# Kernel optimization log

Measured on AMD Instinct MI355X. Metric: run time of the kernel, lower is better.

The kernel has to match this reference:

```python
import jax, jax.numpy as jnp
import numpy as np

D_MODEL = 1024
HEADS = 16
D_HEAD = D_MODEL // HEADS


def setup_inputs() -> dict:
    key = jax.random.key(0)
    ks = jax.random.split(key, 5)
    B, S = 4, 2048
    x = jax.random.normal(ks[0], (B, S, D_MODEL), dtype=jnp.float32)
    # nn.Linear weights are [out, in]; store as [in, out] for x @ W convention
    s_qkv = 1.0 / np.sqrt(D_MODEL)
    w_qkv = jax.random.uniform(ks[1], (D_MODEL, 3 * D_MODEL), jnp.float32, -s_qkv, s_qkv)
    b_qkv = jax.random.uniform(ks[2], (3 * D_MODEL,), jnp.float32, -s_qkv, s_qkv)
    w_proj = jax.random.uniform(ks[3], (D_MODEL, D_MODEL), jnp.float32, -s_qkv, s_qkv)
    b_proj = jax.random.uniform(ks[4], (D_MODEL,), jnp.float32, -s_qkv, s_qkv)
    return {"x": x, "w_qkv": w_qkv, "b_qkv": b_qkv, "w_proj": w_proj, "b_proj": b_proj}


def reference(x, w_qkv, b_qkv, w_proj, b_proj):
    B, S, D = x.shape
    scale = D_HEAD ** (-0.5)
    qkv = x @ w_qkv + b_qkv                        # [B,S,3D]
    qkv = qkv.reshape(B, S, 3, HEADS, D_HEAD)
    qkv = jnp.transpose(qkv, (2, 0, 3, 1, 4))      # [3,B,H,S,dh]
    q, k, v = qkv[0], qkv[1], qkv[2]
    attn = jnp.einsum("bhsd,bhtd->bhst", q, k) * scale
    attn = jax.nn.softmax(attn, axis=-1)
    ctx = jnp.einsum("bhst,bhtd->bhsd", attn, v)   # [B,H,S,dh]
    ctx = jnp.transpose(ctx, (0, 2, 1, 3)).reshape(B, S, D)
    return ctx @ w_proj + b_proj
```

## Files before the change

### kernel.cpp

```cpp
#include <hip/hip_runtime.h>

typedef unsigned short u16;
typedef unsigned int u32;
typedef __attribute__((ext_vector_type(8))) short short8;
typedef __attribute__((ext_vector_type(4))) float f32x4;
typedef __attribute__((ext_vector_type(2))) unsigned int u32x2;

extern "C" __device__ float __ocml_native_exp2_f32(float);

__device__ __forceinline__ u16 f32_to_bf16(float f) {
  u32 u = __builtin_bit_cast(u32, f);
  u += 0x7fffu + ((u >> 16) & 1u);
  return (u16)(u >> 16);
}

__device__ __forceinline__ u32 cvt_pk_bf16(float a, float b) {
  u32 r;
  asm("v_cvt_pk_bf16_f32 %0, %1, %2" : "=v"(r) : "v"(a), "v"(b));
  return r;
}

__device__ __forceinline__ void gload16(const void* g, void* l) {
  __builtin_amdgcn_global_load_lds((const __attribute__((address_space(1))) u32*)g,
                                   (__attribute__((address_space(3))) u32*)l, 16, 0, 0);
}

__global__ __launch_bounds__(256) void prep_kernel(const float* __restrict__ x,
                                                   u16* __restrict__ xb,
                                                   const float* __restrict__ w_qkv,
                                                   u16* __restrict__ wqkvT,
                                                   const float* __restrict__ w_proj,
                                                   u16* __restrict__ wprojT) {
  __shared__ u16 tile[32][33];
  const int bid = blockIdx.x, tid = threadIdx.x;
  if (bid < 4096) {
    int i = bid * 256 + tid;
    const float4* p = (const float4*)x + (size_t)i * 2;
    float4 a = p[0], b = p[1];
    int4 v;
    v.x = (int)f32_to_bf16(a.x) | ((int)f32_to_bf16(a.y) << 16);
    v.y = (int)f32_to_bf16(a.z) | ((int)f32_to_bf16(a.w) << 16);
    v.z = (int)f32_to_bf16(b.x) | ((int)f32_to_bf16(b.y) << 16);
    v.w = (int)f32_to_bf16(b.z) | ((int)f32_to_bf16(b.w) << 16);
    *(int4*)(xb + (size_t)i * 8) = v;
    return;
  }
  const float* in;
  u16* out;
  int bx, by, C;
  if (bid < 7168) {
    int t = bid - 4096;
    bx = t % 96; by = t / 96; C = 3072; in = w_qkv; out = wqkvT;
  } else {
    int t = bid - 7168;
    bx = t % 32; by = t / 32; C = 1024; in = w_proj; out = wprojT;
  }
  const int R = 1024;
  int tx = tid & 31, ty = tid >> 5;
  int c0 = bx * 32, r0 = by * 32;
#pragma unroll
  for (int j = 0; j < 32; j += 8)
    tile[ty + j][tx] = f32_to_bf16(in[(size_t)(r0 + ty + j) * C + c0 + tx]);
  __syncthreads();
#pragma unroll
  for (int j = 0; j < 32; j += 8)
    out[(size_t)(c0 + ty + j) * R + r0 + tx] = tile[tx][ty + j];
}

__global__ __launch_bounds__(512, 2) void gemm256_kernel(
    const u16* __restrict__ A, const u16* __restrict__ Bt, const float* __restrict__ bias,
    u16* __restrict__ qo, u16* __restrict__ ko, u16* __restrict__ vo) {
  __shared__ u16 lds[2][2][2][8192];
  const int tid = threadIdx.x;
  const int lane = tid & 63, w = tid >> 6;
  const int lo = lane & 15, hi = lane >> 4;
  const int wr = w >> 2, wn4 = w & 3;
  const int id = blockIdx.y * gridDim.x + blockIdx.x;
  const int swz = (id & 7) * 48 + (id >> 3);
  const int bn = (swz % 12) * 256, bm = (swz / 12) * 256;
  const int srow4 = lane >> 2;
  const int scol = (lane & 3) ^ ((lane >> 3) & 3);
  const u16* aRow = A + (size_t)(bm + w * 16 + srow4) * 1024 + scol * 8;
  const u16* bRow = Bt + (size_t)(bn + w * 16 + srow4) * 1024 + scol * 8;
  const int achk = (hi ^ ((lo >> 1) & 3)) * 8;
  const int bro = wn4 * 64;

  f32x4 acc[8][4] = {};

#define STG(sdb, sab, shk, tile)                                      \
  if ((tile) < 16) {                                                  \
    const u16* g = ((sab) ? bRow : aRow) + (tile) * 64 + (shk) * 32;  \
    u16* d = &lds[sdb][sab][shk][w * 512];                            \
    gload16(g, d);                                                    \
    gload16(g + 128 * 1024, d + 4096);                                \
  }

#define W8 asm volatile("s_waitcnt vmcnt(8)" ::: "memory")
#define W4 asm volatile("s_waitcnt vmcnt(4)" ::: "memory")
#define W0 asm volatile("s_waitcnt vmcnt(0)" ::: "memory")
#define WN ((void)0)

  STG(0, 0, 0, 0); STG(0, 1, 0, 0); STG(0, 0, 1, 0); STG(0, 1, 1, 0);
  STG(1, 0, 0, 1); STG(1, 1, 0, 1);
  W8;
  __builtin_amdgcn_s_barrier();

#define PHASE(db, MH, KK, sdb, sab, shk, tile, WAITOP)                                           \
  {                                                                                              \
    short8 af[4], bf[4];                                                                         \
    _Pragma("unroll") for (int m4 = 0; m4 < 4; ++m4)                                             \
      af[m4] = *(const short8*)&lds[db][0][KK][(wr * 128 + MH * 64 + m4 * 16 + lo) * 32 + achk]; \
    _Pragma("unroll") for (int ni = 0; ni < 4; ++ni)                                             \
      bf[ni] = *(const short8*)&lds[db][1][KK][(bro + ni * 16 + lo) * 32 + achk];                \
    STG(sdb, sab, shk, tile);                                                                    \
    WAITOP;                                                                                      \
    __builtin_amdgcn_s_barrier();                                                                \
    asm volatile("s_waitcnt lgkmcnt(0)" ::: "memory");                                           \
    __builtin_amdgcn_sched_barrier(0);                                                           \
    __builtin_amdgcn_s_setprio(1);                                                               \
    _Pragma("unroll") for (int m4 = 0; m4 < 4; ++m4)                                             \
      _Pragma("unroll") for (int ni = 0; ni < 4; ++ni)                                           \
        acc[MH * 4 + m4][ni] = __builtin_amdgcn_mfma_f32_16x16x32_bf16(                          \
            af[m4], bf[ni], acc[MH * 4 + m4][ni], 0, 0, 0);                                      \
    __builtin_amdgcn_s_setprio(0);                                                               \
    __builtin_amdgcn_s_barrier();                                                                \
  }

  for (int i = 0; i < 7; ++i) {
    const int t1 = 2 * i + 1, t2 = 2 * i + 2, t3 = 2 * i + 3;
    PHASE(0, 0, 0, 1, 0, 1, t1, WN);
    PHASE(0, 1, 0, 1, 1, 1, t1, W8);
    PHASE(0, 0, 1, 0, 0, 0, t2, WN);
    PHASE(0, 1, 1, 0, 1, 0, t2, W8);
    PHASE(1, 0, 0, 0, 0, 1, t2, WN);
    PHASE(1, 1, 0, 0, 1, 1, t2, W8);
    PHASE(1, 0, 1, 1, 0, 0, t3, WN);
    PHASE(1, 1, 1, 1, 1, 0, t3, W8);
  }
  PHASE(0, 0, 0, 1, 0, 1, 15, WN);
  PHASE(0, 1, 0, 1, 1, 1, 15, W8);
  PHASE(0, 0, 1, 0, 0, 0, 16, WN);
  PHASE(0, 1, 1, 0, 1, 0, 16, W4);
  PHASE(1, 0, 0, 0, 0, 1, 16, WN);
  PHASE(1, 1, 0, 0, 1, 1, 16, W0);
  PHASE(1, 0, 1, 1, 0, 0, 17, WN);
  PHASE(1, 1, 1, 1, 1, 0, 17, WN);
#undef PHASE
#undef STG

  u16* T = &lds[0][0][0][0] + w * 8192;
  const int colbase = bn + wn4 * 64;
  const int part = colbase >> 10;
  const int h = (colbase & 1023) >> 6;
  const int grow0 = bm + wr * 128;
  const int b = grow0 >> 11;
  const int s0 = grow0 & 2047;
  float bv[4];
#pragma unroll
  for (int ni = 0; ni < 4; ++ni) bv[ni] = bias[colbase + ni * 16 + lo];

  if (part < 2) {
    const float scl = (part == 0) ? 0.18033688f : 1.0f;
#pragma unroll
    for (int mi = 0; mi < 8; ++mi)
#pragma unroll
      for (int ni = 0; ni < 4; ++ni) {
        const int col = ni * 16 + lo;
#pragma unroll
        for (int r = 0; r < 4; ++r) {
          const int row = mi * 16 + hi * 4 + r;
          T[row * 64 + (((col >> 3) ^ (row & 7)) * 8) + (col & 7)] =
              f32_to_bf16((acc[mi][ni][r] + bv[ni]) * scl);
        }
      }
    u16* dst = part ? ko : qo;
#pragma unroll
    for (int rr = 0; rr < 16; ++rr) {
      const int row = rr * 8 + (lane >> 3);
      const int c = lane & 7;
      short8 v = *(const short8*)&T[row * 64 + (((c ^ (row & 7)) * 8))];
      *(short8*)&dst[((size_t)(b * 16 + h) * 2048 + s0 + row) * 64 + c * 8] = v;
    }
  } else {
#pragma unroll
    for (int mi = 0; mi < 8; ++mi)
#pragma unroll
      for (int ni = 0; ni < 4; ++ni) {
        const int d = ni * 16 + lo;
        u32x2 wv;
        wv.x = cvt_pk_bf16(acc[mi][ni][0] + bv[ni], acc[mi][ni][1] + bv[ni]);
        wv.y = cvt_pk_bf16(acc[mi][ni][2] + bv[ni], acc[mi][ni][3] + bv[ni]);
        const int chunk = 2 * mi + (hi >> 1);
        *(u32x2*)&T[d * 128 + ((chunk ^ (d & 15)) * 8) + (hi & 1) * 4] = wv;
      }
#pragma unroll
    for (int rr = 0; rr < 16; ++rr) {
      const int u = rr * 64 + lane;
      const int d = u >> 4, c = u & 15;
      short8 v = *(const short8*)&T[d * 128 + ((c ^ (d & 15)) * 8)];
      *(short8*)&vo[((size_t)(b * 16 + h) * 64 + d) * 2048 + s0 + c * 8] = v;
    }
  }
}

template <int MODE>
__global__ __launch_bounds__(256) void gemm_kernel(
    const u16* __restrict__ A, const u16* __restrict__ Bt, const float* __restrict__ bias,
    float* __restrict__ outf, int M, int N, int K) {
  __shared__ u16 Sm[2][2][4096];
  const int tid = threadIdx.x;
  const int id = blockIdx.y * gridDim.x + blockIdx.x;
  const int nwg = gridDim.x * gridDim.y;
  const int swz = (id & 7) * (nwg >> 3) + (id >> 3);
  const int bn = (swz % gridDim.x) * 128;
  const int bm = (swz / gridDim.x) * 128;
  const int lane = tid & 63, wid = tid >> 6;
  const int lo = lane & 15, hi = lane >> 4;
  const int wm = (wid >> 1) * 64, wn = (wid & 1) * 64;
  const int srow = lane >> 2, schk = lane & 3;
  const u16* as0 = A + (size_t)(bm + wid * 32 + srow) * K + schk * 8;
  const u16* bs0 = Bt + (size_t)(bn + wid * 32 + srow) * K + schk * 8;
  const size_t row16 = (size_t)16 * K;

  f32x4 acc[4][4] = {};
  gload16(as0, &Sm[0][0][wid * 1024]);
  gload16(as0 + row16, &Sm[0][0][wid * 1024 + 512]);
  gload16(bs0, &Sm[0][1][wid * 1024]);
  gload16(bs0 + row16, &Sm[0][1][wid * 1024 + 512]);
  int cur = 0;
  for (int k0 = 0; k0 < K; k0 += 32) {
    __syncthreads();
    if (k0 + 32 < K) {
      int nx = cur ^ 1;
      gload16(as0 + k0 + 32, &Sm[nx][0][wid * 1024]);
      gload16(as0 + k0 + 32 + row16, &Sm[nx][0][wid * 1024 + 512]);
      gload16(bs0 + k0 + 32, &Sm[nx][1][wid * 1024]);
      gload16(bs0 + k0 + 32 + row16, &Sm[nx][1][wid * 1024 + 512]);
    }
    const u16* Al = Sm[cur][0];
    const u16* Bl = Sm[cur][1];
    short8 af[4], bfr[4];
#pragma unroll
    for (int mi = 0; mi < 4; ++mi) af[mi] = *(const short8*)&Al[(wm + mi * 16 + lo) * 32 + hi * 8];
#pragma unroll
    for (int ni = 0; ni < 4; ++ni) bfr[ni] = *(const short8*)&Bl[(wn + ni * 16 + lo) * 32 + hi * 8];
#pragma unroll
    for (int mi = 0; mi < 4; ++mi)
#pragma unroll
      for (int ni = 0; ni < 4; ++ni)
        acc[mi][ni] = __builtin_amdgcn_mfma_f32_16x16x32_bf16(af[mi], bfr[ni], acc[mi][ni], 0, 0, 0);
    cur ^= 1;
  }

#pragma unroll
  for (int mi = 0; mi < 4; ++mi)
#pragma unroll
    for (int ni = 0; ni < 4; ++ni) {
      int col = bn + wn + ni * 16 + lo;
      float bvv = bias[col];
#pragma unroll
      for (int r = 0; r < 4; ++r) {
        int row = bm + wm + mi * 16 + hi * 4 + r;
        outf[(size_t)row * N + col] = acc[mi][ni][r] + bvv;
      }
    }
}

__global__ __launch_bounds__(512, 2) void attn_kernel(const u16* __restrict__ Qg,
                                                      const u16* __restrict__ Kg,
                                                      const u16* __restrict__ Vtg,
                                                      u16* __restrict__ ctx) {
  __shared__ u16 KV[2][2][4096];
  __shared__ u16 Pb[8][2048];
  const int tid = threadIdx.x;
  const int lane = tid & 63, wid = tid >> 6;
  const int lo = lane & 15, hi = lane >> 4;
  const int id = blockIdx.y * gridDim.x + blockIdx.x;
  const int swz = (id & 7) * 64 + (id >> 3);
  const int qb = swz & 7, bh = swz >> 3;
  const u16* Qh = Qg + (size_t)bh * (2048 * 64);
  const u16* Kh = Kg + (size_t)bh * (2048 * 64);
  const u16* Vh = Vtg + (size_t)bh * (64 * 2048);

  short8 qf[2][2];
#pragma unroll
  for (int ni = 0; ni < 2; ++ni)
#pragma unroll
    for (int kk = 0; kk < 2; ++kk)
      qf[ni][kk] = *(const short8*)&Qh[(size_t)(qb * 256 + wid * 32 + ni * 16 + lo) * 64 +
                                       kk * 32 + hi * 8];

  const int srow = lane >> 3;
  const int schk = (lane & 7) ^ srow;
  const u16* ksrc = Kh + (size_t)(wid * 8 + srow) * 64 + schk * 8;
  const u16* vsrc = Vh + (size_t)(wid * 8 + srow) * 2048 + schk * 8;

  const short8 ONES = {0x3F80, 0x3F80, 0x3F80, 0x3F80, 0x3F80, 0x3F80, 0x3F80, 0x3F80};
  f32x4 o[2][4] = {};
  f32x4 lst[2] = {};

#define STAGE(buf, kt)                                            \
  do {                                                            \
    gload16(ksrc + (size_t)(kt) * 4096, &KV[buf][0][wid * 512]);  \
    gload16(vsrc + (size_t)(kt) * 64, &KV[buf][1][wid * 512]);    \
  } while (0)

  STAGE(0, 0);
  int cur = 0;
  for (int kt = 0; kt < 32; ++kt) {
    __syncthreads();
    if (kt < 31) STAGE(cur ^ 1, kt + 1);
    const u16* Ks = KV[cur][0];
    const u16* Vs = KV[cur][1];

    f32x4 sa[4][2] = {};
#pragma unroll
    for (int kk = 0; kk < 2; ++kk) {
      short8 kf[4];
#pragma unroll
      for (int mi = 0; mi < 4; ++mi)
        kf[mi] = *(const short8*)&Ks[(mi * 16 + lo) * 64 + (((kk * 4 + hi) ^ (lo & 7)) * 8)];
      __builtin_amdgcn_s_setprio(1);
#pragma unroll
      for (int mi = 0; mi < 4; ++mi)
#pragma unroll
        for (int ni = 0; ni < 2; ++ni)
          sa[mi][ni] = __builtin_amdgcn_mfma_f32_16x16x32_bf16(kf[mi], qf[ni][kk], sa[mi][ni], 0, 0, 0);
      __builtin_amdgcn_s_setprio(0);
    }

#pragma unroll
    for (int mi = 0; mi < 4; ++mi)
#pragma unroll
      for (int ni = 0; ni < 2; ++ni)
#pragma unroll
        for (int r = 0; r < 4; ++r)
          sa[mi][ni][r] = __ocml_native_exp2_f32(sa[mi][ni][r]);

#pragma unroll
    for (int mi = 0; mi < 4; ++mi)
#pragma unroll
      for (int ni = 0; ni < 2; ++ni) {
        u32x2 wv;
        wv.x = cvt_pk_bf16(sa[mi][ni][0], sa[mi][ni][1]);
        wv.y = cvt_pk_bf16(sa[mi][ni][2], sa[mi][ni][3]);
        *(u32x2*)&Pb[wid][(ni * 16 + lo) * 64 +
                          (((2 * mi + (hi >> 1)) ^ (lo & 7)) * 8) + (hi & 1) * 4] = wv;
      }
    asm volatile("s_waitcnt lgkmcnt(0)" ::: "memory");
    __builtin_amdgcn_sched_barrier(0);

#pragma unroll
    for (int kk2 = 0; kk2 < 2; ++kk2) {
      short8 pf[2], vf[4];
#pragma unroll
      for (int qi = 0; qi < 2; ++qi)
        pf[qi] = *(const short8*)&Pb[wid][(qi * 16 + lo) * 64 +
                                          (((4 * kk2 + hi) ^ (lo & 7)) * 8)];
#pragma unroll
      for (int di = 0; di < 4; ++di)
        vf[di] = *(const short8*)&Vs[(di * 16 + lo) * 64 + (((kk2 * 4 + hi) ^ (lo & 7)) * 8)];
      __builtin_amdgcn_s_setprio(1);
#pragma unroll
      for (int qi = 0; qi < 2; ++qi)
        lst[qi] = __builtin_amdgcn_mfma_f32_16x16x32_bf16(pf[qi], ONES, lst[qi], 0, 0, 0);
#pragma unroll
      for (int qi = 0; qi < 2; ++qi)
#pragma unroll
        for (int di = 0; di < 4; ++di)
          o[qi][di] = __builtin_amdgcn_mfma_f32_16x16x32_bf16(pf[qi], vf[di], o[qi][di], 0, 0, 0);
      __builtin_amdgcn_s_setprio(0);
    }
    cur ^= 1;
  }
#undef STAGE

  int b = bh >> 4, h = bh & 15;
#pragma unroll
  for (int qi = 0; qi < 2; ++qi)
#pragma unroll
    for (int r = 0; r < 4; ++r) {
      float inv = __builtin_amdgcn_rcpf(lst[qi][r]);
      int sr = qb * 256 + wid * 32 + qi * 16 + hi * 4 + r;
      u16* crow = ctx + (size_t)(b * 2048 + sr) * 1024 + h * 64;
#pragma unroll
      for (int di = 0; di < 4; ++di) crow[di * 16 + lo] = f32_to_bf16(o[qi][di][r] * inv);
    }
}

extern "C" void kernel_launch(void* const* d_in, const int* in_sizes, int n_in,
                              void* d_out, int out_size, void* d_ws, size_t ws_size,
                              hipStream_t stream) {
  const float* x      = (const float*)d_in[0];
  const float* w_qkv  = (const float*)d_in[1];
  const float* b_qkv  = (const float*)d_in[2];
  const float* w_proj = (const float*)d_in[3];
  const float* b_proj = (const float*)d_in[4];
  float* out = (float*)d_out;
  char* ws = (char*)d_ws;

  u16* xb     = (u16*)(ws);
  u16* wqkvT  = (u16*)(ws + 16777216);
  u16* wprojT = (u16*)(ws + 23068672);
  u16* Vt     = (u16*)(ws + 25165824);
  u16* Q = (u16*)d_out;
  u16* K = Q + 8388608;

  prep_kernel<<<8192, 256, 0, stream>>>(x, xb, w_qkv, wqkvT, w_proj, wprojT);
  gemm256_kernel<<<dim3(12, 32), 512, 0, stream>>>(xb, wqkvT, b_qkv, Q, K, Vt);
  attn_kernel<<<dim3(8, 64), 512, 0, stream>>>(Q, K, Vt, xb);
  gemm_kernel<1><<<dim3(8, 64), 256, 0, stream>>>(xb, wprojT, b_proj, out, 8192, 1024, 1024);
}
```

Baseline: 252.0 us.

## Shrink QKV GEMM tile to 128x256 and reuse pipelined kernel for output projection

Replaces the 256x256 QKV GEMM with a templated 128x256-tile kernel using a simplified 4-phase pipeline. The QKV launch doubles its workgroup count (768 instead of 384) for better CU fill. The same deeply pipelined kernel replaces the simple double-buffered 128x128 output-projection GEMM, which now uses a 128x256 tile. Each wave holds fewer accumulators and A-tile reuse is lower, so more global and LDS traffic is spent per MFMA in exchange for the extra parallelism.

```diff
diff --git a/kernel.cpp b/kernel.cpp
--- a/kernel.cpp
+++ b/kernel.cpp
@@ -67,94 +67,106 @@
     out[(size_t)(c0 + ty + j) * R + r0 + tx] = tile[tx][ty + j];
 }
 
-__global__ __launch_bounds__(512, 2) void gemm256_kernel(
+template <int MODE>
+__global__ __launch_bounds__(512, 1) void gemm8p_kernel(
     const u16* __restrict__ A, const u16* __restrict__ Bt, const float* __restrict__ bias,
-    u16* __restrict__ qo, u16* __restrict__ ko, u16* __restrict__ vo) {
-  __shared__ u16 lds[2][2][2][8192];
+    u16* __restrict__ qo, u16* __restrict__ ko, u16* __restrict__ vo,
+    float* __restrict__ outf) {
+  __shared__ u16 shm[49152];
   const int tid = threadIdx.x;
   const int lane = tid & 63, w = tid >> 6;
   const int lo = lane & 15, hi = lane >> 4;
   const int wr = w >> 2, wn4 = w & 3;
   const int id = blockIdx.y * gridDim.x + blockIdx.x;
-  const int swz = (id & 7) * 48 + (id >> 3);
-  const int bn = (swz % 12) * 256, bm = (swz / 12) * 256;
+  const int nwg = gridDim.x * gridDim.y;
+  const int swz = (id & 7) * (nwg >> 3) + (id >> 3);
+  const int bn = (swz % gridDim.x) * 256;
+  const int bm = (swz / gridDim.x) * 128;
   const int srow4 = lane >> 2;
   const int scol = (lane & 3) ^ ((lane >> 3) & 3);
   const u16* aRow = A + (size_t)(bm + w * 16 + srow4) * 1024 + scol * 8;
-  const u16* bRow = Bt + (size_t)(bn + w * 16 + srow4) * 1024 + scol * 8;
+  const u16* bRow = Bt + (size_t)(bn + w * 32 + srow4) * 1024 + scol * 8;
+  const u16* bRow2 = bRow + 16 * 1024;
   const int achk = (hi ^ ((lo >> 1) & 3)) * 8;
-  const int bro = wn4 * 64;
-
-  f32x4 acc[8][4] = {};
-
-#define STG(sdb, sab, shk, tile)                                      \
-  if ((tile) < 16) {                                                  \
-    const u16* g = ((sab) ? bRow : aRow) + (tile) * 64 + (shk) * 32;  \
-    u16* d = &lds[sdb][sab][shk][w * 512];                            \
-    gload16(g, d);                                                    \
-    gload16(g + 128 * 1024, d + 4096);                                \
-  }
-
-#define W8 asm volatile("s_waitcnt vmcnt(8)" ::: "memory")
-#define W4 asm volatile("s_waitcnt vmcnt(4)" ::: "memory")
+
+  f32x4 acc[4][4] = {};
+
+#define AL(db, kk) (shm + ((db) * 2 + (kk)) * 4096)
+#define BL(db, kk) (shm + 16384 + ((db) * 2 + (kk)) * 8192)
+#define STG(sdb, shk, tile)                                \
+  if ((tile) < 16) {                                       \
+    const int off = (tile) * 64 + (shk) * 32;              \
+    gload16(aRow + off, AL(sdb, shk) + w * 512);           \
+    gload16(bRow + off, BL(sdb, shk) + w * 1024);          \
+    gload16(bRow2 + off, BL(sdb, shk) + w * 1024 + 512);   \
+  }
+#define W6 asm volatile("s_waitcnt vmcnt(6)" ::: "memory")
+#define W3 asm volatile("s_waitcnt vmcnt(3)" ::: "memory")
 #define W0 asm volatile("s_waitcnt vmcnt(0)" ::: "memory")
 #define WN ((void)0)
 
-  STG(0, 0, 0, 0); STG(0, 1, 0, 0); STG(0, 0, 1, 0); STG(0, 1, 1, 0);
-  STG(1, 0, 0, 1); STG(1, 1, 0, 1);
-  W8;
+  STG(0, 0, 0); STG(0, 1, 0); STG(1, 0, 1);
+  W6;
   __builtin_amdgcn_s_barrier();
 
-#define PHASE(db, MH, KK, sdb, sab, shk, tile, WAITOP)                                           \
-  {                                                                                              \
-    short8 af[4], bf[4];                                                                         \
-    _Pragma("unroll") for (int m4 = 0; m4 < 4; ++m4)                                             \
-      af[m4] = *(const short8*)&lds[db][0][KK][(wr * 128 + MH * 64 + m4 * 16 + lo) * 32 + achk]; \
-    _Pragma("unroll") for (int ni = 0; ni < 4; ++ni)                                             \
-      bf[ni] = *(const short8*)&lds[db][1][KK][(bro + ni * 16 + lo) * 32 + achk];                \
-    STG(sdb, sab, shk, tile);                                                                    \
-    WAITOP;                                                                                      \
-    __builtin_amdgcn_s_barrier();                                                                \
-    asm volatile("s_waitcnt lgkmcnt(0)" ::: "memory");                                           \
-    __builtin_amdgcn_sched_barrier(0);                                                           \
-    __builtin_amdgcn_s_setprio(1);                                                               \
-    _Pragma("unroll") for (int m4 = 0; m4 < 4; ++m4)                                             \
-      _Pragma("unroll") for (int ni = 0; ni < 4; ++ni)                                           \
-        acc[MH * 4 + m4][ni] = __builtin_amdgcn_mfma_f32_16x16x32_bf16(                          \
-            af[m4], bf[ni], acc[MH * 4 + m4][ni], 0, 0, 0);                                      \
-    __builtin_amdgcn_s_setprio(0);                                                               \
-    __builtin_amdgcn_s_barrier();                                                                \
-  }
-
-  for (int i = 0; i < 7; ++i) {
-    const int t1 = 2 * i + 1, t2 = 2 * i + 2, t3 = 2 * i + 3;
-    PHASE(0, 0, 0, 1, 0, 1, t1, WN);
-    PHASE(0, 1, 0, 1, 1, 1, t1, W8);
-    PHASE(0, 0, 1, 0, 0, 0, t2, WN);
-    PHASE(0, 1, 1, 0, 1, 0, t2, W8);
-    PHASE(1, 0, 0, 0, 0, 1, t2, WN);
-    PHASE(1, 1, 0, 0, 1, 1, t2, W8);
-    PHASE(1, 0, 1, 1, 0, 0, t3, WN);
-    PHASE(1, 1, 1, 1, 1, 0, t3, W8);
-  }
-  PHASE(0, 0, 0, 1, 0, 1, 15, WN);
-  PHASE(0, 1, 0, 1, 1, 1, 15, W8);
-  PHASE(0, 0, 1, 0, 0, 0, 16, WN);
-  PHASE(0, 1, 1, 0, 1, 0, 16, W4);
-  PHASE(1, 0, 0, 0, 0, 1, 16, WN);
-  PHASE(1, 1, 0, 0, 1, 1, 16, W0);
-  PHASE(1, 0, 1, 1, 0, 0, 17, WN);
-  PHASE(1, 1, 1, 1, 1, 0, 17, WN);
+#define PHASE(db, KK, sdb, shk, stile, WAITOP)                                        \
+  {                                                                                   \
+    short8 af[4], bf[4];                                                              \
+    _Pragma("unroll") for (int m4 = 0; m4 < 4; ++m4)                                  \
+      af[m4] = *(const short8*)&AL(db, KK)[(wr * 64 + m4 * 16 + lo) * 32 + achk];     \
+    _Pragma("unroll") for (int ni = 0; ni < 4; ++ni)                                  \
+      bf[ni] = *(const short8*)&BL(db, KK)[(wn4 * 64 + ni * 16 + lo) * 32 + achk];    \
+    STG(sdb, shk, stile);                                                             \
+    WAITOP;                                                                           \
+    __builtin_amdgcn_s_barrier();                                                     \
+    asm volatile("s_waitcnt lgkmcnt(0)" ::: "memory");                                \
+    __builtin_amdgcn_sched_barrier(0);                                                \
+    __builtin_amdgcn_s_setprio(1);                                                    \
+    _Pragma("unroll") for (int m4 = 0; m4 < 4; ++m4)                                  \
+      _Pragma("unroll") for (int ni = 0; ni < 4; ++ni)                                \
+        acc[m4][ni] = __builtin_amdgcn_mfma_f32_16x16x32_bf16(                        \
+            af[m4], bf[ni], acc[m4][ni], 0, 0, 0);                                    \
+    __builtin_amdgcn_s_setprio(0);                                                    \
+    __builtin_amdgcn_s_barrier();                                                     \
+  }
+
+  for (int tt = 0; tt < 7; ++tt) {
+    PHASE(0, 0, 1, 1, 2 * tt + 1, W6);
+    PHASE(0, 1, 0, 0, 2 * tt + 2, W6);
+    PHASE(1, 0, 0, 1, 2 * tt + 2, W6);
+    PHASE(1, 1, 1, 0, 2 * tt + 3, W6);
+  }
+  PHASE(0, 0, 1, 1, 15, W6);
+  PHASE(0, 1, 0, 0, 16, W3);
+  PHASE(1, 0, 0, 1, 16, W0);
+  PHASE(1, 1, 1, 0, 17, WN);
 #undef PHASE
 #undef STG
-
-  u16* T = &lds[0][0][0][0] + w * 8192;
+#undef AL
+#undef BL
+
+  if (MODE == 1) {
+#pragma unroll
+    for (int mi = 0; mi < 4; ++mi)
+#pragma unroll
+      for (int ni = 0; ni < 4; ++ni) {
+        int col = bn + wn4 * 64 + ni * 16 + lo;
+        float bvv = bias[col];
+#pragma unroll
+        for (int r = 0; r < 4; ++r) {
+          int row = bm + wr * 64 + mi * 16 + hi * 4 + r;
+          outf[(size_t)row * 1024 + col] = acc[mi][ni][r] + bvv;
+        }
+      }
+    return;
+  }
+
+  u16* T = shm + w * 4096;
   const int colbase = bn + wn4 * 64;
   const int part = colbase >> 10;
   const int h = (colbase & 1023) >> 6;
-  const int grow0 = bm + wr * 128;
-  const int b = grow0 >> 11;
-  const int s0 = grow0 & 2047;
+  const int b = bm >> 11;
+  const int s0 = (bm & 2047) + wr * 64;
   float bv[4];
 #pragma unroll
   for (int ni = 0; ni < 4; ++ni) bv[ni] = bias[colbase + ni * 16 + lo];
@@ -162,7 +174,7 @@
   if (part < 2) {
     const float scl = (part == 0) ? 0.18033688f : 1.0f;
 #pragma unroll
-    for (int mi = 0; mi < 8; ++mi)
+    for (int mi = 0; mi < 4; ++mi)
 #pragma unroll
       for (int ni = 0; ni < 4; ++ni) {
         const int col = ni * 16 + lo;
@@ -175,15 +187,15 @@
       }
     u16* dst = part ? ko : qo;
 #pragma unroll
-    for (int rr = 0; rr < 16; ++rr) {
+    for (int rr = 0; rr < 8; ++rr) {
       const int row = rr * 8 + (lane >> 3);
       const int c = lane & 7;
-      short8 v = *(const short8*)&T[row * 64 + (((c ^ (row & 7)) * 8))];
+      short8 v = *(const short8*)&T[row * 64 + ((c ^ (row & 7)) * 8)];
       *(short8*)&dst[((size_t)(b * 16 + h) * 2048 + s0 + row) * 64 + c * 8] = v;
     }
   } else {
 #pragma unroll
-    for (int mi = 0; mi < 8; ++mi)
+    for (int mi = 0; mi < 4; ++mi)
 #pragma unroll
       for (int ni = 0; ni < 4; ++ni) {
         const int d = ni * 16 + lo;
@@ -191,79 +203,16 @@
         wv.x = cvt_pk_bf16(acc[mi][ni][0] + bv[ni], acc[mi][ni][1] + bv[ni]);
         wv.y = cvt_pk_bf16(acc[mi][ni][2] + bv[ni], acc[mi][ni][3] + bv[ni]);
         const int chunk = 2 * mi + (hi >> 1);
-        *(u32x2*)&T[d * 128 + ((chunk ^ (d & 15)) * 8) + (hi & 1) * 4] = wv;
+        *(u32x2*)&T[d * 64 + ((chunk ^ (d & 7)) * 8) + (hi & 1) * 4] = wv;
       }
 #pragma unroll
-    for (int rr = 0; rr < 16; ++rr) {
+    for (int rr = 0; rr < 8; ++rr) {
       const int u = rr * 64 + lane;
-      const int d = u >> 4, c = u & 15;
-      short8 v = *(const short8*)&T[d * 128 + ((c ^ (d & 15)) * 8)];
+      const int d = u >> 3, c = u & 7;
+      short8 v = *(const short8*)&T[d * 64 + ((c ^ (d & 7)) * 8)];
       *(short8*)&vo[((size_t)(b * 16 + h) * 64 + d) * 2048 + s0 + c * 8] = v;
     }
   }
-}
-
-template <int MODE>
-__global__ __launch_bounds__(256) void gemm_kernel(
-    const u16* __restrict__ A, const u16* __restrict__ Bt, const float* __restrict__ bias,
-    float* __restrict__ outf, int M, int N, int K) {
-  __shared__ u16 Sm[2][2][4096];
-  const int tid = threadIdx.x;
-  const int id = blockIdx.y * gridDim.x + blockIdx.x;
-  const int nwg = gridDim.x * gridDim.y;
-  const int swz = (id & 7) * (nwg >> 3) + (id >> 3);
-  const int bn = (swz % gridDim.x) * 128;
-  const int bm = (swz / gridDim.x) * 128;
-  const int lane = tid & 63, wid = tid >> 6;
-  const int lo = lane & 15, hi = lane >> 4;
-  const int wm = (wid >> 1) * 64, wn = (wid & 1) * 64;
-  const int srow = lane >> 2, schk = lane & 3;
-  const u16* as0 = A + (size_t)(bm + wid * 32 + srow) * K + schk * 8;
-  const u16* bs0 = Bt + (size_t)(bn + wid * 32 + srow) * K + schk * 8;
-  const size_t row16 = (size_t)16 * K;
-
-  f32x4 acc[4][4] = {};
-  gload16(as0, &Sm[0][0][wid * 1024]);
-  gload16(as0 + row16, &Sm[0][0][wid * 1024 + 512]);
-  gload16(bs0, &Sm[0][1][wid * 1024]);
-  gload16(bs0 + row16, &Sm[0][1][wid * 1024 + 512]);
-  int cur = 0;
-  for (int k0 = 0; k0 < K; k0 += 32) {
-    __syncthreads();
-    if (k0 + 32 < K) {
-      int nx = cur ^ 1;
-      gload16(as0 + k0 + 32, &Sm[nx][0][wid * 1024]);
-      gload16(as0 + k0 + 32 + row16, &Sm[nx][0][wid * 1024 + 512]);
-      gload16(bs0 + k0 + 32, &Sm[nx][1][wid * 1024]);
-      gload16(bs0 + k0 + 32 + row16, &Sm[nx][1][wid * 1024 + 512]);
-    }
-    const u16* Al = Sm[cur][0];
-    const u16* Bl = Sm[cur][1];
-    short8 af[4], bfr[4];
-#pragma unroll
-    for (int mi = 0; mi < 4; ++mi) af[mi] = *(const short8*)&Al[(wm + mi * 16 + lo) * 32 + hi * 8];
-#pragma unroll
-    for (int ni = 0; ni < 4; ++ni) bfr[ni] = *(const short8*)&Bl[(wn + ni * 16 + lo) * 32 + hi * 8];
-#pragma unroll
-    for (int mi = 0; mi < 4; ++mi)
-#pragma unroll
-      for (int ni = 0; ni < 4; ++ni)
-        acc[mi][ni] = __builtin_amdgcn_mfma_f32_16x16x32_bf16(af[mi], bfr[ni], acc[mi][ni], 0, 0, 0);
-    cur ^= 1;
-  }
-
-#pragma unroll
-  for (int mi = 0; mi < 4; ++mi)
-#pragma unroll
-    for (int ni = 0; ni < 4; ++ni) {
-      int col = bn + wn + ni * 16 + lo;
-      float bvv = bias[col];
-#pragma unroll
-      for (int r = 0; r < 4; ++r) {
-        int row = bm + wm + mi * 16 + hi * 4 + r;
-        outf[(size_t)row * N + col] = acc[mi][ni][r] + bvv;
-      }
-    }
 }
 
 __global__ __launch_bounds__(512, 2) void attn_kernel(const u16* __restrict__ Qg,
@@ -407,7 +356,8 @@
   u16* K = Q + 8388608;
 
   prep_kernel<<<8192, 256, 0, stream>>>(x, xb, w_qkv, wqkvT, w_proj, wprojT);
-  gemm256_kernel<<<dim3(12, 32), 512, 0, stream>>>(xb, wqkvT, b_qkv, Q, K, Vt);
+  gemm8p_kernel<0><<<dim3(12, 64), 512, 0, stream>>>(xb, wqkvT, b_qkv, Q, K, Vt, nullptr);
   attn_kernel<<<dim3(8, 64), 512, 0, stream>>>(Q, K, Vt, xb);
-  gemm_kernel<1><<<dim3(8, 64), 256, 0, stream>>>(xb, wprojT, b_proj, out, 8192, 1024, 1024);
-}
+  gemm8p_kernel<1><<<dim3(4, 64), 512, 0, stream>>>(xb, wprojT, b_proj,
+                                                    nullptr, nullptr, nullptr, out);
+}
```

Result: faster. 240.7 us (-4.5%).
